# Optimization experiments

Hardware: AMD Instinct MI355X
Metric: run time of the kernel (lower is better)

The kernel has to match this reference:

```python
import jax, jax.numpy as jnp
import numpy as np

N_BOTTLENECK = 256  # must be a power of two for the butterfly network


def butterfly_ortho(x, theta, first_output_entry_positive=False):
    """FFT-like butterfly of Givens rotations over the last dim (size n, power of 2).
    Stage s pairs indices (i, i + 2^s); each pair gets one rotation angle.
    theta has (n/2)*log2(n) entries, consumed stage by stage.
    """
    n = x.shape[-1]
    stages = int(np.log2(n))
    idx = 0
    for s in range(stages):
        stride = 1 << s
        nb = n // (2 * stride)
        th = theta[idx: idx + n // 2].reshape(nb, stride)
        idx += n // 2
        xr = x.reshape(-1, nb, 2, stride)  # [B, blocks, half, offset]
        a, b = xr[:, :, 0, :], xr[:, :, 1, :]
        c, sn = jnp.cos(th), jnp.sin(th)
        a2 = c * a - sn * b
        b2 = sn * a + c * b
        x = jnp.stack([a2, b2], axis=2).reshape(-1, n)
    if first_output_entry_positive:
        # convention flag: force sign of first output entry non-negative
        x = x.at[:, 0].set(jnp.abs(x[:, 0]))
    return x


def setup_inputs() -> dict:
    key = jax.random.key(0)
    ks = jax.random.split(key, 12)
    dims = [4096, 1024, 256, 1024, 4096]
    B = 16384

    def w(k, i, o):
        return (jax.random.normal(k, (i, o), dtype=jnp.float32) * (1.0 / np.sqrt(i)))

    inp = {
        "x": jax.random.normal(ks[0], (B, dims[0]), dtype=jnp.float32),
        "enc_w0": w(ks[1], dims[0], dims[1]),
        "enc_b0": jnp.zeros((dims[1],), jnp.float32),
        "enc_w1": w(ks[2], dims[1], dims[2]),
        "enc_b1": jnp.zeros((dims[2],), jnp.float32),
        "theta": jax.random.normal(ks[3], ((dims[2] // 2) * int(np.log2(dims[2])),), dtype=jnp.float32),
        "dec_w0": w(ks[4], dims[2], dims[3]),
        "dec_b0": jnp.zeros((dims[3],), jnp.float32),
        "out_w": w(ks[5], dims[3], dims[4]),
        "out_b": jnp.zeros((dims[4],), jnp.float32),
    }
    return inp


def reference(x, enc_w0, enc_b0, enc_w1, enc_b1, theta, dec_w0, dec_b0, out_w, out_b):
    # encoder: Linear + ReLU stack
    h = jax.nn.relu(x @ enc_w0 + enc_b0)
    h = jax.nn.relu(h @ enc_w1 + enc_b1)
    # orthogonal butterfly network at the bottleneck
    h = butterfly_ortho(h, theta, first_output_entry_positive=False)
    # decoder: Linear + ReLU stack, then plain Linear output layer
    h = jax.nn.relu(h @ dec_w0 + dec_b0)
    out = h @ out_w + out_b
    return out
```

## Files before the change

kernel.cpp:

```cpp
#include <hip/hip_runtime.h>

typedef __attribute__((ext_vector_type(8))) short short8v;
typedef __attribute__((ext_vector_type(4))) float f32x4;
typedef __attribute__((ext_vector_type(4))) unsigned int uint4v;
typedef __attribute__((ext_vector_type(4))) float float4v;

__device__ __forceinline__ unsigned short f2bf(float f) {
  union { float f; unsigned u; } v; v.f = f;
  unsigned r = v.u + 0x7fffu + ((v.u >> 16) & 1u);
  return (unsigned short)(r >> 16);
}
__device__ __forceinline__ float bf2f(unsigned short h) {
  union { unsigned u; float f; } v; v.u = ((unsigned)h) << 16;
  return v.f;
}
__device__ __forceinline__ unsigned pack2(float a, float b) {
  return (unsigned)f2bf(a) | ((unsigned)f2bf(b) << 16);
}

__device__ __forceinline__ void gload_lds16(const void* g, void* l) {
  __builtin_amdgcn_global_load_lds(
      (const __attribute__((address_space(1))) void*)g,
      (__attribute__((address_space(3))) void*)l, 16, 0, 0);
}

#define SBAR() __builtin_amdgcn_s_barrier()
#define LGKM(n) do { asm volatile("s_waitcnt lgkmcnt(" #n ")" ::: "memory"); \
                     __builtin_amdgcn_sched_barrier(0); } while (0)
#define VMW(n) asm volatile("s_waitcnt vmcnt(" #n ")" ::: "memory")

__global__ void f32_to_bf16(const float* __restrict__ in, unsigned short* __restrict__ out,
                            size_t n8) {
  size_t i = (size_t)blockIdx.x * blockDim.x + threadIdx.x;
  const size_t stride = (size_t)gridDim.x * blockDim.x;
  for (; i < n8; i += stride) {
    const float4v* p = (const float4v*)(in + i * 8);
    float4v a = p[0], b = p[1];
    uint4v r;
    r.x = pack2(a.x, a.y); r.y = pack2(a.z, a.w);
    r.z = pack2(b.x, b.y); r.w = pack2(b.z, b.w);
    *(uint4v*)(out + i * 8) = r;
  }
}

__global__ void transpose_bf16(const float* __restrict__ W, unsigned short* __restrict__ WT,
                               int K, int N) {
  __shared__ float t[32][33];
  const int kb = blockIdx.x * 32, nb = blockIdx.y * 32;
  const int tx = threadIdx.x, ty = threadIdx.y;
  #pragma unroll
  for (int y = 0; y < 4; ++y)
    t[ty + y*8][tx] = W[(size_t)(kb + ty + y*8) * N + nb + tx];
  __syncthreads();
  #pragma unroll
  for (int y = 0; y < 4; ++y) {
    const int n = nb + ty + y*8;
    WT[(size_t)n * K + kb + tx] = f2bf(t[tx][ty + y*8]);
  }
}

__global__ void trig_kernel(const float* __restrict__ theta, float* __restrict__ ct,
                            float* __restrict__ st, int n) {
  const int i = blockIdx.x * 256 + threadIdx.x;
  if (i < n) {
    float s, c;
    sincosf(theta[i], &s, &c);
    ct[i] = c; st[i] = s;
  }
}

__global__ void butterfly_kernel(const unsigned short* __restrict__ X,
                                 unsigned short* __restrict__ Y,
                                 const float* __restrict__ ct, const float* __restrict__ st) {
  __shared__ float L[2][256];
  const int tid = threadIdx.x;
  const size_t base = (size_t)blockIdx.x * 512;
  const unsigned v = *(const unsigned*)(X + base + tid * 2);
  const int r = tid >> 7;
  const int col = (tid * 2) & 255;
  L[r][col]     = bf2f((unsigned short)(v & 0xffffu));
  L[r][col + 1] = bf2f((unsigned short)(v >> 16));
  __syncthreads();
  const int p = tid & 127;
  #pragma unroll
  for (int s = 0; s < 8; ++s) {
    const int stride = 1 << s;
    const int t = p & (stride - 1);
    const int i = ((p >> s) << (s + 1)) + t;
    const int j = i + stride;
    const float c  = ct[s * 128 + p];
    const float sn = st[s * 128 + p];
    const float a = L[r][i], b = L[r][j];
    L[r][i] = c * a - sn * b;
    L[r][j] = sn * a + c * b;
    __syncthreads();
  }
  const unsigned lo = f2bf(L[r][col]);
  const unsigned hi = f2bf(L[r][col + 1]);
  *(unsigned*)(Y + base + tid * 2) = lo | (hi << 16);
}

template<bool RELU, bool OUT_F32>
__global__ __launch_bounds__(256) void gemm_kernel(
    const unsigned short* __restrict__ A, const unsigned short* __restrict__ BT,
    const float* __restrict__ bias, void* __restrict__ Cp,
    int M, int N, int K)
{
  __shared__ __align__(16) unsigned short As[128 * 32];
  __shared__ __align__(16) unsigned short Bs[128 * 32];
  const int tid = threadIdx.x;
  const int lane = tid & 63;
  const int w = tid >> 6;
  const int wm = w >> 1, wn = w & 1;
  const int n0 = blockIdx.x * 128;
  const int m0 = blockIdx.y * 128;
  const int g4 = lane >> 4;
  const int ml = lane & 15;

  f32x4 acc[4][4];
  #pragma unroll
  for (int i = 0; i < 4; ++i)
    #pragma unroll
    for (int n = 0; n < 4; ++n)
      #pragma unroll
      for (int e = 0; e < 4; ++e)
        acc[i][n][e] = 0.0f;

  const int nkt = K >> 5;
  const int srow = w * 32 + (lane >> 2);
  const int scol = (lane & 3) * 8;

  for (int kt = 0; kt < nkt; ++kt) {
    const int k0 = kt << 5;
    #pragma unroll
    for (int q = 0; q < 2; ++q) {
      const unsigned short* gb = BT + (size_t)(n0 + srow + q * 16) * K + k0 + scol;
      gload_lds16(gb, Bs + w * 1024 + q * 512);
      const unsigned short* ga = A + (size_t)(m0 + srow + q * 16) * K + k0 + scol;
      gload_lds16(ga, As + w * 1024 + q * 512);
    }
    __syncthreads();
    short8v af[4], bf[4];
    #pragma unroll
    for (int i = 0; i < 4; ++i)
      af[i] = *(const short8v*)(As + (wm * 64 + i * 16 + ml) * 32 + g4 * 8);
    #pragma unroll
    for (int n = 0; n < 4; ++n)
      bf[n] = *(const short8v*)(Bs + (wn * 64 + n * 16 + ml) * 32 + g4 * 8);
    #pragma unroll
    for (int i = 0; i < 4; ++i)
      #pragma unroll
      for (int n = 0; n < 4; ++n)
        acc[i][n] = __builtin_amdgcn_mfma_f32_16x16x32_bf16(af[i], bf[n], acc[i][n], 0, 0, 0);
    __syncthreads();
  }
  #pragma unroll
  for (int n = 0; n < 4; ++n) {
    const int col = n0 + wn * 64 + n * 16 + ml;
    const float bv = bias[col];
    #pragma unroll
    for (int i = 0; i < 4; ++i) {
      const int rowb = m0 + wm * 64 + i * 16 + g4 * 4;
      #pragma unroll
      for (int r = 0; r < 4; ++r) {
        float v = acc[i][n][r] + bv;
        if constexpr (RELU) v = fmaxf(v, 0.0f);
        if constexpr (OUT_F32)
          ((float*)Cp)[(size_t)(rowb + r) * N + col] = v;
        else
          ((unsigned short*)Cp)[(size_t)(rowb + r) * N + col] = f2bf(v);
      }
    }
  }
}

template<int MI0, int NI0>
__device__ __forceinline__ void mfma_quad(f32x4 (&acc)[8][4], const short8v (&a)[4][2],
                                          const short8v (&b)[2][2]) {
  __builtin_amdgcn_s_setprio(1);
  #pragma unroll
  for (int mi = 0; mi < 4; ++mi)
    #pragma unroll
    for (int ni = 0; ni < 2; ++ni) {
      acc[MI0+mi][NI0+ni] = __builtin_amdgcn_mfma_f32_16x16x32_bf16(
          a[mi][0], b[ni][0], acc[MI0+mi][NI0+ni], 0, 0, 0);
      acc[MI0+mi][NI0+ni] = __builtin_amdgcn_mfma_f32_16x16x32_bf16(
          a[mi][1], b[ni][1], acc[MI0+mi][NI0+ni], 0, 0, 0);
    }
  __builtin_amdgcn_s_setprio(0);
}

template<bool RELU, bool OUT_F32>
__global__ __launch_bounds__(512, 2) void gemm256(
    const unsigned short* __restrict__ A, const unsigned short* __restrict__ BT,
    const float* __restrict__ bias, void* __restrict__ Cp,
    int M, int N, int K)
{
  __shared__ __align__(16) unsigned char lds[131072];
  const int tid = threadIdx.x;
  const int lane = tid & 63, w = tid >> 6;
  const int wm = w >> 2, wn = w & 3;
  const int ml = lane & 15, g4 = lane >> 4;

  const int nx = gridDim.x;
  const int nwg = nx * (int)gridDim.y;
  const int bid = blockIdx.y * nx + blockIdx.x;
  const int cpx = nwg >> 3;
  const int swz = (bid & 7) * cpx + (bid >> 3);
  const int n0 = (swz % nx) * 256;
  const int m0 = (swz / nx) * 256;

  const int rloc = w * 8 + (lane >> 3);
  const int scol = ((lane & 7) ^ (lane >> 3)) * 8;
  const int ldst = w * 1024;

  const int off0 = (g4 * 16) ^ ((ml & 7) << 4);
  const int aoff = (wm * 128 + ml) * 128 + off0;
  const int boff = (wn * 64 + ml) * 128 + off0;

  const int NT = K >> 6;
  const int NJ = NT >> 1;

  f32x4 acc[8][4];
  #pragma unroll
  for (int mi = 0; mi < 8; ++mi)
    #pragma unroll
    for (int ni = 0; ni < 4; ++ni)
      #pragma unroll
      for (int e = 0; e < 4; ++e)
        acc[mi][ni][e] = 0.0f;

  auto stA = [&](int d, int h, int t) {
    const unsigned short* g0 = A + (size_t)(m0 + h * 128 + rloc) * K + t * 64 + scol;
    unsigned char* l0 = lds + d * 65536 + h * 16384 + ldst;
    gload_lds16(g0, l0);
    gload_lds16(g0 + (size_t)64 * K, l0 + 8192);
  };
  auto stB = [&](int d, int h, int t) {
    const unsigned short* g0 = BT + (size_t)(n0 + h * 128 + rloc) * K + t * 64 + scol;
    unsigned char* l0 = lds + d * 65536 + 32768 + h * 16384 + ldst;
    gload_lds16(g0, l0);
    gload_lds16(g0 + (size_t)64 * K, l0 + 8192);
  };
  auto rdA = [&](short8v (&dst)[4][2], int d, int mh) {
    #pragma unroll
    for (int mi = 0; mi < 4; ++mi) {
      const int ab = d * 65536 + aoff + (mh * 4 + mi) * 2048;
      dst[mi][0] = *(const short8v*)(lds + ab);
      dst[mi][1] = *(const short8v*)(lds + (ab ^ 64));
    }
  };
  auto rdB = [&](short8v (&dst)[2][2], int d, int nh) {
    #pragma unroll
    for (int ni = 0; ni < 2; ++ni) {
      const int bb = d * 65536 + 32768 + boff + (nh * 2 + ni) * 2048;
      dst[ni][0] = *(const short8v*)(lds + bb);
      dst[ni][1] = *(const short8v*)(lds + (bb ^ 64));
    }
  };

  short8v A0[4][2], A1[4][2], B0[2][2], B1[2][2];

  stB(0, 0, 0); stB(0, 1, 0); stA(0, 0, 0); stA(0, 1, 0);
  stB(1, 0, 1); stB(1, 1, 1);
  VMW(4);
  SBAR();
  rdA(A0, 0, 0); rdB(B0, 0, 0);

  for (int j = 0; j < NJ; ++j) {
    const int t1 = 2 * j + 1;
    const int t2 = (2 * j + 2 < NT) ? 2 * j + 2 : NT - 1;
    const int t3 = (2 * j + 3 < NT) ? 2 * j + 3 : NT - 1;

    rdB(B1, 0, 1);
    stA(1, 0, t1);
    SBAR(); LGKM(4);
    mfma_quad<0, 0>(acc, A0, B0);
    SBAR();
    rdA(A1, 0, 1);
    stA(1, 1, t1);
    SBAR(); LGKM(8);
    mfma_quad<0, 2>(acc, A0, B1);
    SBAR();
    stB(0, 0, t2);
    SBAR(); LGKM(0);
    mfma_quad<4, 0>(acc, A1, B0);
    VMW(2);
    SBAR();
    rdA(A0, 1, 0); rdB(B0, 1, 0);
    stB(0, 1, t2);
    SBAR(); LGKM(12);
    mfma_quad<4, 2>(acc, A1, B1);
    SBAR();
    rdB(B1, 1, 1);
    stA(0, 0, t2);
    SBAR(); LGKM(4);
    mfma_quad<0, 0>(acc, A0, B0);
    SBAR();
    rdA(A1, 1, 1);
    stA(0, 1, t2);
    SBAR(); LGKM(8);
    mfma_quad<0, 2>(acc, A0, B1);
    SBAR();
    stB(1, 0, t3);
    SBAR(); LGKM(0);
    mfma_quad<4, 0>(acc, A1, B0);
    VMW(2);
    SBAR();
    rdA(A0, 0, 0); rdB(B0, 0, 0);
    stB(1, 1, t3);
    SBAR(); LGKM(12);
    mfma_quad<4, 2>(acc, A1, B1);
    SBAR();
  }

  #pragma unroll
  for (int ni = 0; ni < 4; ++ni) {
    const int col = n0 + wn * 64 + ni * 16 + ml;
    const float bv = bias[col];
    #pragma unroll
    for (int mi = 0; mi < 8; ++mi) {
      const int rowb = m0 + wm * 128 + mi * 16 + g4 * 4;
      #pragma unroll
      for (int r = 0; r < 4; ++r) {
        float v = acc[mi][ni][r] + bv;
        if constexpr (RELU) v = fmaxf(v, 0.0f);
        if constexpr (OUT_F32)
          ((float*)Cp)[(size_t)(rowb + r) * N + col] = v;
        else
          ((unsigned short*)Cp)[(size_t)(rowb + r) * N + col] = f2bf(v);
      }
    }
  }
}

extern "C" void kernel_launch(void* const* d_in, const int* in_sizes, int n_in,
                              void* d_out, int out_size, void* d_ws, size_t ws_size,
                              hipStream_t stream) {
  const float* x      = (const float*)d_in[0];
  const float* enc_w0 = (const float*)d_in[1];
  const float* enc_b0 = (const float*)d_in[2];
  const float* enc_w1 = (const float*)d_in[3];
  const float* enc_b1 = (const float*)d_in[4];
  const float* theta  = (const float*)d_in[5];
  const float* dec_w0 = (const float*)d_in[6];
  const float* dec_b0 = (const float*)d_in[7];
  const float* out_w  = (const float*)d_in[8];
  const float* out_b  = (const float*)d_in[9];
  float* out = (float*)d_out;

  char* ws = (char*)d_ws;
  unsigned short* xb  = (unsigned short*)(ws);
  unsigned short* wt0 = (unsigned short*)(ws + 134217728);
  unsigned short* wt1 = (unsigned short*)(ws + 142606336);
  unsigned short* wt2 = (unsigned short*)(ws + 143130624);
  unsigned short* wt3 = (unsigned short*)(ws + 143654912);
  unsigned short* h1  = (unsigned short*)(ws + 152043520);
  unsigned short* h2  = (unsigned short*)(ws + 185597952);
  unsigned short* h2b = (unsigned short*)(ws + 193986560);
  unsigned short* h3  = h1;
  float* ct = (float*)(ws + 202375168);
  float* st = ct + 1024;

  const int B = 16384;

  f32_to_bf16<<<2048, 256, 0, stream>>>(x, xb, (size_t)B * 4096 / 8);
  transpose_bf16<<<dim3(4096/32, 1024/32), dim3(32, 8), 0, stream>>>(enc_w0, wt0, 4096, 1024);
  transpose_bf16<<<dim3(1024/32,  256/32), dim3(32, 8), 0, stream>>>(enc_w1, wt1, 1024, 256);
  transpose_bf16<<<dim3( 256/32, 1024/32), dim3(32, 8), 0, stream>>>(dec_w0, wt2, 256, 1024);
  transpose_bf16<<<dim3(1024/32, 4096/32), dim3(32, 8), 0, stream>>>(out_w,  wt3, 1024, 4096);
  trig_kernel<<<4, 256, 0, stream>>>(theta, ct, st, 1024);

  gemm256<true,  false><<<dim3(1024/256, B/256), 512, 0, stream>>>(xb, wt0, enc_b0, h1, B, 1024, 4096);
  gemm_kernel<true,  false><<<dim3( 256/128, B/128), 256, 0, stream>>>(h1, wt1, enc_b1, h2, B, 256, 1024);
  butterfly_kernel<<<B/2, 256, 0, stream>>>(h2, h2b, ct, st);
  gemm_kernel<true,  false><<<dim3(1024/128, B/128), 256, 0, stream>>>(h2b, wt2, dec_b0, h3, B, 1024, 256);
  gemm256<false, true ><<<dim3(4096/256, B/256), 512, 0, stream>>>(h3, wt3, out_b, out, B, 4096, 1024);
}
```

Measured before the change: 475.8 us.

## Split LDS fragment reads by K-half and restage the GEMM pipeline

The gemm256 main loop now reads A and B fragments from LDS in two K-halves and waits on partial lgkmcnt between two half-size MFMA batches, so matrix work can start before all fragment reads land. Each phase reloads its B fragments instead of carrying them across phases, and the vmcnt wait moves. Separately, the fp32-to-bf16 conversion uses nontemporal loads and the fp32 output stores use nontemporal stores to reduce cache pollution. The new schedule issues more LDS reads and more waits per tile, which may add overhead or disturb the existing global-load and LDS overlap.

Result: faster. 394.0 us, median of 2 (-17.2%).

```diff
diff --git a/kernel.cpp b/kernel.cpp
--- a/kernel.cpp
+++ b/kernel.cpp
@@ -25,6 +25,7 @@
 }
 
 #define SBAR() __builtin_amdgcn_s_barrier()
+#define SCHED0() __builtin_amdgcn_sched_barrier(0)
 #define LGKM(n) do { asm volatile("s_waitcnt lgkmcnt(" #n ")" ::: "memory"); \
                      __builtin_amdgcn_sched_barrier(0); } while (0)
 #define VMW(n) asm volatile("s_waitcnt vmcnt(" #n ")" ::: "memory")
@@ -35,7 +36,8 @@
   const size_t stride = (size_t)gridDim.x * blockDim.x;
   for (; i < n8; i += stride) {
     const float4v* p = (const float4v*)(in + i * 8);
-    float4v a = p[0], b = p[1];
+    float4v a = __builtin_nontemporal_load(p);
+    float4v b = __builtin_nontemporal_load(p + 1);
     uint4v r;
     r.x = pack2(a.x, a.y); r.y = pack2(a.z, a.w);
     r.z = pack2(b.x, b.y); r.w = pack2(b.z, b.w);
@@ -166,7 +168,7 @@
         float v = acc[i][n][r] + bv;
         if constexpr (RELU) v = fmaxf(v, 0.0f);
         if constexpr (OUT_F32)
-          ((float*)Cp)[(size_t)(rowb + r) * N + col] = v;
+          __builtin_nontemporal_store(v, &((float*)Cp)[(size_t)(rowb + r) * N + col]);
         else
           ((unsigned short*)Cp)[(size_t)(rowb + r) * N + col] = f2bf(v);
       }
@@ -175,18 +177,15 @@
 }
 
 template<int MI0, int NI0>
-__device__ __forceinline__ void mfma_quad(f32x4 (&acc)[8][4], const short8v (&a)[4][2],
-                                          const short8v (&b)[2][2]) {
+__device__ __forceinline__ void mfma8(f32x4 (&acc)[8][4], const short8v (&a)[4],
+                                      const short8v (&b)[2]) {
   __builtin_amdgcn_s_setprio(1);
   #pragma unroll
   for (int mi = 0; mi < 4; ++mi)
     #pragma unroll
-    for (int ni = 0; ni < 2; ++ni) {
+    for (int ni = 0; ni < 2; ++ni)
       acc[MI0+mi][NI0+ni] = __builtin_amdgcn_mfma_f32_16x16x32_bf16(
-          a[mi][0], b[ni][0], acc[MI0+mi][NI0+ni], 0, 0, 0);
-      acc[MI0+mi][NI0+ni] = __builtin_amdgcn_mfma_f32_16x16x32_bf16(
-          a[mi][1], b[ni][1], acc[MI0+mi][NI0+ni], 0, 0, 0);
-    }
+          a[mi], b[ni], acc[MI0+mi][NI0+ni], 0, 0, 0);
   __builtin_amdgcn_s_setprio(0);
 }
 
@@ -242,75 +241,106 @@
     gload_lds16(g0, l0);
     gload_lds16(g0 + (size_t)64 * K, l0 + 8192);
   };
-  auto rdA = [&](short8v (&dst)[4][2], int d, int mh) {
-    #pragma unroll
-    for (int mi = 0; mi < 4; ++mi) {
-      const int ab = d * 65536 + aoff + (mh * 4 + mi) * 2048;
-      dst[mi][0] = *(const short8v*)(lds + ab);
-      dst[mi][1] = *(const short8v*)(lds + (ab ^ 64));
-    }
-  };
-  auto rdB = [&](short8v (&dst)[2][2], int d, int nh) {
-    #pragma unroll
-    for (int ni = 0; ni < 2; ++ni) {
-      const int bb = d * 65536 + 32768 + boff + (nh * 2 + ni) * 2048;
-      dst[ni][0] = *(const short8v*)(lds + bb);
-      dst[ni][1] = *(const short8v*)(lds + (bb ^ 64));
-    }
-  };
-
-  short8v A0[4][2], A1[4][2], B0[2][2], B1[2][2];
+  auto rdA0 = [&](short8v (&dst)[4], int d, int mh) {
+    #pragma unroll
+    for (int mi = 0; mi < 4; ++mi)
+      dst[mi] = *(const short8v*)(lds + d * 65536 + aoff + (mh * 4 + mi) * 2048);
+  };
+  auto rdA1 = [&](short8v (&dst)[4], int d, int mh) {
+    #pragma unroll
+    for (int mi = 0; mi < 4; ++mi)
+      dst[mi] = *(const short8v*)(lds + ((d * 65536 + aoff + (mh * 4 + mi) * 2048) ^ 64));
+  };
+  auto rdB0 = [&](short8v (&dst)[2], int d, int nh) {
+    #pragma unroll
+    for (int ni = 0; ni < 2; ++ni)
+      dst[ni] = *(const short8v*)(lds + d * 65536 + 32768 + boff + (nh * 2 + ni) * 2048);
+  };
+  auto rdB1 = [&](short8v (&dst)[2], int d, int nh) {
+    #pragma unroll
+    for (int ni = 0; ni < 2; ++ni)
+      dst[ni] = *(const short8v*)(lds + ((d * 65536 + 32768 + boff + (nh * 2 + ni) * 2048) ^ 64));
+  };
+
+  short8v aR_0[4], aR_1[4], aS_0[4], aS_1[4];
+  short8v bR0_0[2], bR0_1[2], bR1_0[2], bR1_1[2];
 
   stB(0, 0, 0); stB(0, 1, 0); stA(0, 0, 0); stA(0, 1, 0);
   stB(1, 0, 1); stB(1, 1, 1);
   VMW(4);
   SBAR();
-  rdA(A0, 0, 0); rdB(B0, 0, 0);
 
   for (int j = 0; j < NJ; ++j) {
     const int t1 = 2 * j + 1;
     const int t2 = (2 * j + 2 < NT) ? 2 * j + 2 : NT - 1;
     const int t3 = (2 * j + 3 < NT) ? 2 * j + 3 : NT - 1;
 
-    rdB(B1, 0, 1);
+    rdB0(bR0_0, 0, 0); rdA0(aR_0, 0, 0);
+    SCHED0();
+    rdB1(bR0_1, 0, 0); rdA1(aR_1, 0, 0);
     stA(1, 0, t1);
+    SBAR(); LGKM(6);
+    mfma8<0, 0>(acc, aR_0, bR0_0);
+    LGKM(0);
+    mfma8<0, 0>(acc, aR_1, bR0_1);
+    SBAR();
+    rdB0(bR1_0, 0, 1);
+    SCHED0();
+    rdB1(bR1_1, 0, 1);
+    stA(1, 1, t1);
+    SBAR(); LGKM(2);
+    mfma8<0, 2>(acc, aR_0, bR1_0);
+    LGKM(0);
+    mfma8<0, 2>(acc, aR_1, bR1_1);
+    SBAR();
+    rdA0(aS_0, 0, 1);
+    SCHED0();
+    rdA1(aS_1, 0, 1);
+    stB(0, 0, t2);
     SBAR(); LGKM(4);
-    mfma_quad<0, 0>(acc, A0, B0);
-    SBAR();
-    rdA(A1, 0, 1);
-    stA(1, 1, t1);
-    SBAR(); LGKM(8);
-    mfma_quad<0, 2>(acc, A0, B1);
-    SBAR();
-    stB(0, 0, t2);
-    SBAR(); LGKM(0);
-    mfma_quad<4, 0>(acc, A1, B0);
-    VMW(2);
-    SBAR();
-    rdA(A0, 1, 0); rdB(B0, 1, 0);
+    mfma8<4, 0>(acc, aS_0, bR0_0);
+    LGKM(0);
+    mfma8<4, 0>(acc, aS_1, bR0_1);
+    SBAR();
     stB(0, 1, t2);
-    SBAR(); LGKM(12);
-    mfma_quad<4, 2>(acc, A1, B1);
-    SBAR();
-    rdB(B1, 1, 1);
+    SBAR();
+    mfma8<4, 2>(acc, aS_0, bR1_0);
+    mfma8<4, 2>(acc, aS_1, bR1_1);
+    VMW(4);
+    SBAR();
+
+    rdB0(bR0_0, 1, 0); rdA0(aR_0, 1, 0);
+    SCHED0();
+    rdB1(bR0_1, 1, 0); rdA1(aR_1, 1, 0);
     stA(0, 0, t2);
+    SBAR(); LGKM(6);
+    mfma8<0, 0>(acc, aR_0, bR0_0);
+    LGKM(0);
+    mfma8<0, 0>(acc, aR_1, bR0_1);
+    SBAR();
+    rdB0(bR1_0, 1, 1);
+    SCHED0();
+    rdB1(bR1_1, 1, 1);
+    stA(0, 1, t2);
+    SBAR(); LGKM(2);
+    mfma8<0, 2>(acc, aR_0, bR1_0);
+    LGKM(0);
+    mfma8<0, 2>(acc, aR_1, bR1_1);
+    SBAR();
+    rdA0(aS_0, 1, 1);
+    SCHED0();
+    rdA1(aS_1, 1, 1);
+    stB(1, 0, t3);
     SBAR(); LGKM(4);
-    mfma_quad<0, 0>(acc, A0, B0);
-    SBAR();
-    rdA(A1, 1, 1);
-    stA(0, 1, t2);
-    SBAR(); LGKM(8);
-    mfma_quad<0, 2>(acc, A0, B1);
-    SBAR();
-    stB(1, 0, t3);
-    SBAR(); LGKM(0);
-    mfma_quad<4, 0>(acc, A1, B0);
-    VMW(2);
-    SBAR();
-    rdA(A0, 0, 0); rdB(B0, 0, 0);
+    mfma8<4, 0>(acc, aS_0, bR0_0);
+    LGKM(0);
+    mfma8<4, 0>(acc, aS_1, bR0_1);
+    SBAR();
     stB(1, 1, t3);
-    SBAR(); LGKM(12);
-    mfma_quad<4, 2>(acc, A1, B1);
+    SBAR();
+    mfma8<4, 2>(acc, aS_0, bR1_0);
+    mfma8<4, 2>(acc, aS_1, bR1_1);
+    VMW(4);
     SBAR();
   }
 
@@ -326,7 +356,7 @@
         float v = acc[mi][ni][r] + bv;
         if constexpr (RELU) v = fmaxf(v, 0.0f);
         if constexpr (OUT_F32)
-          ((float*)Cp)[(size_t)(rowb + r) * N + col] = v;
+          __builtin_nontemporal_store(v, &((float*)Cp)[(size_t)(rowb + r) * N + col]);
         else
           ((unsigned short*)Cp)[(size_t)(rowb + r) * N + col] = f2bf(v);
       }
```
